# Optimization experiments

Hardware: AMD Instinct MI355X
Metric: run time of the kernel (lower is better)

## Reference

```python
import jax, jax.numpy as jnp
import numpy as np
from jax import lax

BLOCK_SIZE = 7
KEEP_PROB = 0.9


def _dropblock_mask(noise, feat_size, dtype):
    # gamma: per-pixel center-drop probability (DropBlock paper eq.)
    pad = (BLOCK_SIZE - 1) // 2
    gamma = (1.0 - KEEP_PROB) / (BLOCK_SIZE ** 2) * (feat_size ** 2) / ((feat_size - BLOCK_SIZE + 1) ** 2)
    centers = (noise < gamma).astype(dtype)  # [C, H, W] Bernoulli(gamma) centers
    # outOfRegion: zero centers within `pad` of any border
    border = jnp.zeros((feat_size, feat_size), dtype=dtype).at[pad:feat_size - pad, pad:feat_size - pad].set(1.0)
    centers = centers * border
    # getRegion: dilate each center into a block_size x block_size square == max-pool, stride 1, SAME
    dilated = lax.reduce_window(centers, jnp.array(0.0, dtype), lax.max,
                                (1, BLOCK_SIZE, BLOCK_SIZE), (1, 1, 1), 'SAME')
    # torch.where(region == 1, 0, 1)
    return 1.0 - dilated  # [C, H, W]


def setup_inputs() -> dict:
    key = jax.random.key(0)
    k1, k2 = jax.random.split(key)
    x = jax.random.normal(k1, (32, 256, 64, 64), dtype=jnp.float32)
    noise = jax.random.uniform(k2, (256, 64, 64), dtype=jnp.float32)
    return {"x": x, "noise": noise}


def reference(x, noise):
    feat_size = x.shape[-1]
    mask = _dropblock_mask(noise, feat_size, x.dtype)  # [C, H, W], shared across batch
    return x * mask[None]
```

## Files before the change

kernel.cpp:

```cpp
#include <hip/hip_runtime.h>


constexpr int C = 256;
constexpr int B = 32;
constexpr int BATCH_PER_BLOCK = 4;

__global__ __launch_bounds__(256)
void dropblock_kernel(const float* __restrict__ x,
                      const float* __restrict__ noise,
                      float* __restrict__ out) {
    const int c = blockIdx.x;
    const int slice = blockIdx.y;

    __shared__ unsigned long long rowS[64];
    __shared__ unsigned long long dil[64];

    const int tid = threadIdx.x;
    const int lane = tid & 63;
    const int wv = tid >> 6;

    const double gamma = (1.0 - 0.9) / (7.0 * 7.0) * (64.0 * 64.0) / (58.0 * 58.0);

    const float* nc = noise + (size_t)c * 4096;
    for (int h = wv; h < 64; h += 4) {
        float v = nc[h * 64 + lane];
        bool center = ((double)v < gamma) && (h >= 3) && (h <= 60)
                                          && (lane >= 3) && (lane <= 60);
        unsigned long long bits = __ballot(center);
        unsigned long long t = bits | (bits << 1) | (bits >> 1);
        unsigned long long s = t | (t << 2) | (t >> 2);
        if (lane == 0) rowS[h] = s;
    }
    __syncthreads();

    if (tid < 64) {
        int lo = tid - 3; if (lo < 0) lo = 0;
        int hi = tid + 3; if (hi > 63) hi = 63;
        unsigned long long d = 0;
        for (int hh = lo; hh <= hi; ++hh) d |= rowS[hh];
        dil[tid] = d;
    }
    __syncthreads();

    const int b0 = slice * BATCH_PER_BLOCK;
    #pragma unroll
    for (int bb = 0; bb < BATCH_PER_BLOCK; ++bb) {
        const size_t img = (size_t)(b0 + bb) * C + c;
        const float4* xi = (const float4*)x + img * 1024;
        float4* oi = (float4*)out + img * 1024;
        #pragma unroll
        for (int k = 0; k < 4; ++k) {
            const int i = tid + k * 256;
            float4 v = xi[i];
            const int h = i >> 4;
            const int w0 = (i & 15) << 2;
            const unsigned long long bits = dil[h];
            v.x = ((bits >> (w0 + 0)) & 1ull) ? 0.0f : v.x;
            v.y = ((bits >> (w0 + 1)) & 1ull) ? 0.0f : v.y;
            v.z = ((bits >> (w0 + 2)) & 1ull) ? 0.0f : v.z;
            v.w = ((bits >> (w0 + 3)) & 1ull) ? 0.0f : v.w;
            oi[i] = v;
        }
    }
}

extern "C" void kernel_launch(void* const* d_in, const int* in_sizes, int n_in,
                              void* d_out, int out_size, void* d_ws, size_t ws_size,
                              hipStream_t stream) {
    const float* x = (const float*)d_in[0];
    const float* noise = (const float*)d_in[1];
    float* out = (float*)d_out;

    dim3 grid(C, B / BATCH_PER_BLOCK);
    dropblock_kernel<<<grid, 256, 0, stream>>>(x, noise, out);
}
```

Measured before the change: 51.69 us.

## Split mask build and apply into two kernels with grid-stride nontemporal streaming

Mask construction moves into a separate small kernel that writes per-channel row bitmasks to workspace. A second grid-stride kernel then streams x with vector loads and nontemporal stores, reading bitmasks from global memory. This stops each block from recomputing the mask from noise and decouples the streaming layout from the channel grid. The cost is an extra kernel launch, a global round-trip for the mask, and a dependency on out_size being in the element units the code assumes.

```diff
diff --git a/kernel.cpp b/kernel.cpp
--- a/kernel.cpp
+++ b/kernel.cpp
@@ -2,18 +2,14 @@
 
 
 constexpr int C = 256;
-constexpr int B = 32;
-constexpr int BATCH_PER_BLOCK = 4;
+
+typedef float f32x4 __attribute__((ext_vector_type(4)));
 
 __global__ __launch_bounds__(256)
-void dropblock_kernel(const float* __restrict__ x,
-                      const float* __restrict__ noise,
-                      float* __restrict__ out) {
+void mask_kernel(const float* __restrict__ noise,
+                 unsigned long long* __restrict__ maskbits) {
     const int c = blockIdx.x;
-    const int slice = blockIdx.y;
-
     __shared__ unsigned long long rowS[64];
-    __shared__ unsigned long long dil[64];
 
     const int tid = threadIdx.x;
     const int lane = tid & 63;
@@ -38,29 +34,24 @@
         int hi = tid + 3; if (hi > 63) hi = 63;
         unsigned long long d = 0;
         for (int hh = lo; hh <= hi; ++hh) d |= rowS[hh];
-        dil[tid] = d;
+        maskbits[c * 64 + tid] = d;
     }
-    __syncthreads();
+}
 
-    const int b0 = slice * BATCH_PER_BLOCK;
-    #pragma unroll
-    for (int bb = 0; bb < BATCH_PER_BLOCK; ++bb) {
-        const size_t img = (size_t)(b0 + bb) * C + c;
-        const float4* xi = (const float4*)x + img * 1024;
-        float4* oi = (float4*)out + img * 1024;
-        #pragma unroll
-        for (int k = 0; k < 4; ++k) {
-            const int i = tid + k * 256;
-            float4 v = xi[i];
-            const int h = i >> 4;
-            const int w0 = (i & 15) << 2;
-            const unsigned long long bits = dil[h];
-            v.x = ((bits >> (w0 + 0)) & 1ull) ? 0.0f : v.x;
-            v.y = ((bits >> (w0 + 1)) & 1ull) ? 0.0f : v.y;
-            v.z = ((bits >> (w0 + 2)) & 1ull) ? 0.0f : v.z;
-            v.w = ((bits >> (w0 + 3)) & 1ull) ? 0.0f : v.w;
-            oi[i] = v;
-        }
+__global__ __launch_bounds__(256)
+void apply_kernel(const f32x4* __restrict__ x,
+                  const unsigned long long* __restrict__ maskbits,
+                  f32x4* __restrict__ out, int n4) {
+    const int stride = gridDim.x * 256;
+    for (int i = blockIdx.x * 256 + threadIdx.x; i < n4; i += stride) {
+        f32x4 v = x[i];
+        const unsigned long long b = maskbits[(i >> 4) & 16383];
+        const int w0 = (i & 15) << 2;
+        v.x = ((b >> (w0 + 0)) & 1ull) ? 0.0f : v.x;
+        v.y = ((b >> (w0 + 1)) & 1ull) ? 0.0f : v.y;
+        v.z = ((b >> (w0 + 2)) & 1ull) ? 0.0f : v.z;
+        v.w = ((b >> (w0 + 3)) & 1ull) ? 0.0f : v.w;
+        __builtin_nontemporal_store(v, &out[i]);
     }
 }
 
@@ -70,7 +61,11 @@
     const float* x = (const float*)d_in[0];
     const float* noise = (const float*)d_in[1];
     float* out = (float*)d_out;
+    unsigned long long* maskbits = (unsigned long long*)d_ws;
 
-    dim3 grid(C, B / BATCH_PER_BLOCK);
-    dropblock_kernel<<<grid, 256, 0, stream>>>(x, noise, out);
+    mask_kernel<<<C, 256, 0, stream>>>(noise, maskbits);
+
+    const int n4 = out_size / 4;
+    apply_kernel<<<2048, 256, 0, stream>>>((const f32x4*)x, maskbits,
+                                           (f32x4*)out, n4);
 }
```

Measured after the change: 54.53 us. 5.5% more time.

## Batch all loads before stores and halve images per block

Applied to the files above, without the earlier changes.

Each block now handles 2 batch images instead of 4, so the grid doubles to 256x16 blocks. Mask nibbles are extracted once per thread into registers. All eight vector loads are issued together before any compute or store, which raises memory-level parallelism per thread. The trade is that each block recomputes the noise-based mask twice as often across the grid, and register use goes up.

```diff
diff --git a/kernel.cpp b/kernel.cpp
--- a/kernel.cpp
+++ b/kernel.cpp
@@ -2,8 +2,8 @@
 
 
 constexpr int C = 256;
-constexpr int B = 32;
-constexpr int BATCH_PER_BLOCK = 4;
+
+typedef float f32x4 __attribute__((ext_vector_type(4)));
 
 __global__ __launch_bounds__(256)
 void dropblock_kernel(const float* __restrict__ x,
@@ -42,26 +42,40 @@
     }
     __syncthreads();
 
-    const int b0 = slice * BATCH_PER_BLOCK;
+    const int b0 = slice * 2;
+    const size_t img0 = (size_t)(b0 + 0) * C + c;
+    const size_t img1 = (size_t)(b0 + 1) * C + c;
+    const f32x4* x0 = (const f32x4*)x + img0 * 1024;
+    const f32x4* x1 = (const f32x4*)x + img1 * 1024;
+    f32x4* o0 = (f32x4*)out + img0 * 1024;
+    f32x4* o1 = (f32x4*)out + img1 * 1024;
+
+    unsigned m[4];
     #pragma unroll
-    for (int bb = 0; bb < BATCH_PER_BLOCK; ++bb) {
-        const size_t img = (size_t)(b0 + bb) * C + c;
-        const float4* xi = (const float4*)x + img * 1024;
-        float4* oi = (float4*)out + img * 1024;
-        #pragma unroll
-        for (int k = 0; k < 4; ++k) {
-            const int i = tid + k * 256;
-            float4 v = xi[i];
-            const int h = i >> 4;
-            const int w0 = (i & 15) << 2;
-            const unsigned long long bits = dil[h];
-            v.x = ((bits >> (w0 + 0)) & 1ull) ? 0.0f : v.x;
-            v.y = ((bits >> (w0 + 1)) & 1ull) ? 0.0f : v.y;
-            v.z = ((bits >> (w0 + 2)) & 1ull) ? 0.0f : v.z;
-            v.w = ((bits >> (w0 + 3)) & 1ull) ? 0.0f : v.w;
-            oi[i] = v;
-        }
+    for (int k = 0; k < 4; ++k) {
+        const int i = tid + k * 256;
+        m[k] = (unsigned)(dil[i >> 4] >> ((i & 15) << 2)) & 0xF;
     }
+
+    f32x4 v[8];
+    #pragma unroll
+    for (int k = 0; k < 4; ++k) v[k]     = x0[tid + k * 256];
+    #pragma unroll
+    for (int k = 0; k < 4; ++k) v[k + 4] = x1[tid + k * 256];
+
+    #pragma unroll
+    for (int k = 0; k < 8; ++k) {
+        const unsigned mk = m[k & 3];
+        v[k].x = (mk & 1u) ? 0.0f : v[k].x;
+        v[k].y = (mk & 2u) ? 0.0f : v[k].y;
+        v[k].z = (mk & 4u) ? 0.0f : v[k].z;
+        v[k].w = (mk & 8u) ? 0.0f : v[k].w;
+    }
+
+    #pragma unroll
+    for (int k = 0; k < 4; ++k) o0[tid + k * 256] = v[k];
+    #pragma unroll
+    for (int k = 0; k < 4; ++k) o1[tid + k * 256] = v[k + 4];
 }
 
 extern "C" void kernel_launch(void* const* d_in, const int* in_sizes, int n_in,
@@ -71,6 +85,6 @@
     const float* noise = (const float*)d_in[1];
     float* out = (float*)d_out;
 
-    dim3 grid(C, B / BATCH_PER_BLOCK);
+    dim3 grid(C, 16);
     dropblock_kernel<<<grid, 256, 0, stream>>>(x, noise, out);
 }
```

New measurement: 52.38 us. About the same (+1.3%).
